# Performance work log

Measured on AMD Instinct MI355X. Metric: run time of the kernel, lower is better.

The kernel has to match this reference:

```python
import jax, jax.numpy as jnp
import numpy as np

T, B, D, H, F, E = 2048, 2, 1024, 16, 4096, 8
HD = D // H


def layer_norm(x, g, b, eps=1e-5):
    m = x.mean(-1, keepdims=True)
    v = ((x - m) ** 2).mean(-1, keepdims=True)
    return (x - m) * jax.lax.rsqrt(v + eps) * g + b


def setup_inputs() -> dict:
    key = jax.random.key(0)
    ks = jax.random.split(key, 24)
    s = 0.02
    inp = {
        "x": jax.random.normal(ks[0], (T, B, D), jnp.float32),
        # self-attention (fairseq MultiheadAttention)
        "Wq": jax.random.normal(ks[1], (D, D), jnp.float32) * s,
        "bq": jnp.zeros((D,), jnp.float32),
        "Wk": jax.random.normal(ks[2], (D, D), jnp.float32) * s,
        "bk": jnp.zeros((D,), jnp.float32),
        "Wv": jax.random.normal(ks[3], (D, D), jnp.float32) * s,
        "bv": jnp.zeros((D,), jnp.float32),
        "Wo": jax.random.normal(ks[4], (D, D), jnp.float32) * s,
        "bo": jnp.zeros((D,), jnp.float32),
        "ln1_g": jnp.ones((D,), jnp.float32),
        "ln1_b": jnp.zeros((D,), jnp.float32),
        "ln2_g": jnp.ones((D,), jnp.float32),
        "ln2_b": jnp.zeros((D,), jnp.float32),
        # MoE: expert_centroids Linear(D -> E, bias=False) => weight [E, D]
        "cent": jax.random.normal(ks[5], (E, D), jnp.float32) * s,
        # per-expert MoESublayer params (base_sublayers=1)
        "e_ln_g": jnp.ones((E, D), jnp.float32),
        "e_ln_b": jnp.zeros((E, D), jnp.float32),
        "e_W1": jax.random.normal(ks[6], (E, D, F), jnp.float32) * s,
        "e_b1": jnp.zeros((E, F), jnp.float32),
        "e_W2": jax.random.normal(ks[7], (E, F, D), jnp.float32) * s,
        "e_b2": jnp.zeros((E, D), jnp.float32),
    }
    return inp


def reference(x, Wq, bq, Wk, bk, Wv, bv, Wo, bo, ln1_g, ln1_b, ln2_g, ln2_b,
              cent, e_ln_g, e_ln_b, e_W1, e_b1, e_W2, e_b2):
    # ---- self-attention block (pre-norm, causal) ----
    res = x  # [T,B,D]
    h = layer_norm(x, ln1_g, ln1_b)
    q = ((h @ Wq) + bq) * (HD ** -0.5)
    k = h @ Wk + bk
    v = h @ Wv + bv
    q = q.reshape(T, B, H, HD)
    k = k.reshape(T, B, H, HD)
    v = v.reshape(T, B, H, HD)
    scores = jnp.einsum('tbhd,sbhd->bhts', q, k)
    causal = jnp.tril(jnp.ones((T, T), bool))
    scores = jnp.where(causal, scores, -1e9)
    p = jax.nn.softmax(scores, axis=-1)
    a = jnp.einsum('bhts,sbhd->tbhd', p, v).reshape(T, B, D)
    x = res + (a @ Wo + bo)

    # ---- MoE block (pre-norm) ----
    res = x
    h = layer_norm(x, ln2_g, ln2_b)
    # MoELayer: transpose(0,1) then flatten -> [B*T, D] token-major by batch
    xs = h.transpose(1, 0, 2).reshape(B * T, D)
    logits = xs.astype(jnp.float32) @ cent.T  # fp32 gating, [N,E]
    assign = jnp.argmax(logits, axis=-1)      # greedy top-1 routing

    # single-device semantics: All2All identity; sort + inverse-sort cancel,
    # so out[t] = expert_{assign[t]}(xs[t]). Compute each expert densely and select.
    def sublayer(g, b, W1, b1, W2, b2):
        hh = jax.nn.relu(layer_norm(xs, g, b) @ W1 + b1)  # [N,F]
        return xs + hh @ W2 + b2                          # internal residual

    ys = jax.vmap(sublayer)(e_ln_g, e_ln_b, e_W1, e_b1, e_W2, e_b2)  # [E,N,D]
    moe_out = jnp.take_along_axis(ys, assign[None, :, None], axis=0)[0]  # [N,D]
    moe_out = moe_out.reshape(B, T, D).transpose(1, 0, 2)  # back to [T,B,D]

    return res + moe_out
```

## Files before the change

kernel.cpp:

```cpp
#include <hip/hip_runtime.h>
#include <hip/hip_bf16.h>
#include <math.h>

#define T_ 2048
#define B_ 2
#define D_ 1024
#define H_ 16
#define F_ 4096
#define E_ 8
#define N_ 4096
#define HD_ 64
#define PADROWS 5120

typedef __attribute__((ext_vector_type(8))) short short8_t;
typedef __attribute__((ext_vector_type(4))) float f32x4_t;
typedef __attribute__((ext_vector_type(16))) float f32x16_t;
typedef __attribute__((ext_vector_type(4))) unsigned u32x4_t;

__device__ __forceinline__ unsigned short f2bf(float f) {
    union { float f; unsigned u; } a; a.f = f;
    unsigned r = a.u + 0x7FFFu + ((a.u >> 16) & 1u);
    return (unsigned short)(r >> 16);
}

__device__ __forceinline__ unsigned cvtpk(float lo, float hi) {
    unsigned r;
    asm("v_cvt_pk_bf16_f32 %0, %1, %2" : "=v"(r) : "v"(lo), "v"(hi));
    return r;
}

__device__ __forceinline__ void glds16(const unsigned short* g, unsigned short* l) {
    __builtin_amdgcn_global_load_lds(
        (const __attribute__((address_space(1))) void*)g,
        (__attribute__((address_space(3))) void*)l, 16, 0, 0);
}

__device__ __forceinline__ void blockReduce2(float& a, float& b, float* sm) {
    #pragma unroll
    for (int m = 32; m; m >>= 1) { a += __shfl_xor(a, m); b += __shfl_xor(b, m); }
    const int w = threadIdx.x >> 6, l = threadIdx.x & 63;
    __syncthreads();
    if (l == 0) { sm[w] = a; sm[8 + w] = b; }
    __syncthreads();
    a = sm[0] + sm[1] + sm[2] + sm[3];
    b = sm[8] + sm[9] + sm[10] + sm[11];
}

__global__ __launch_bounds__(256) void k_transpose(const float* __restrict__ in,
                                                   unsigned short* __restrict__ out,
                                                   int R, int C) {
    __shared__ float tile[32][33];
    const int c0 = blockIdx.x * 32, r0 = blockIdx.y * 32;
    const size_t base = (size_t)blockIdx.z * R * C;
    in += base; out += base;
    const int tx = threadIdx.x & 31, ty = threadIdx.x >> 5;
    #pragma unroll
    for (int i = 0; i < 32; i += 8)
        tile[ty + i][tx] = in[(size_t)(r0 + ty + i) * C + c0 + tx];
    __syncthreads();
    #pragma unroll
    for (int i = 0; i < 32; i += 8)
        out[(size_t)(c0 + ty + i) * R + r0 + tx] = f2bf(tile[tx][ty + i]);
}

__global__ __launch_bounds__(256) void k_transpose_v(const unsigned short* __restrict__ in,
                                                     unsigned short* __restrict__ out) {
    const int bh = blockIdx.x;
    const int t0 = blockIdx.y * 128;
    const int tid = threadIdx.x;
    const int hd = tid & 63;
    const size_t ib = (size_t)bh * T_ * HD_;
    const size_t ob = (size_t)bh * HD_ * T_;
    for (int tb = tid >> 6; tb < 16; tb += 4) {
        const int t = t0 + tb * 8;
        short8_t v;
        #pragma unroll
        for (int k = 0; k < 8; ++k)
            v[k] = (short)in[ib + (size_t)(t + k) * HD_ + hd];
        *(short8_t*)(out + ob + (size_t)hd * T_ + t) = v;
    }
}

__global__ __launch_bounds__(256) void k_ln(const float* __restrict__ x,
                                            const float* __restrict__ g,
                                            const float* __restrict__ b,
                                            unsigned short* __restrict__ out) {
    __shared__ float sm[16];
    const int row = blockIdx.x, tid = threadIdx.x;
    const float4 v = *(const float4*)(x + (size_t)row * D_ + tid * 4);
    float s1 = v.x + v.y + v.z + v.w;
    float s2 = v.x * v.x + v.y * v.y + v.z * v.z + v.w * v.w;
    blockReduce2(s1, s2, sm);
    const float mean = s1 * (1.f / D_);
    const float inv  = rsqrtf(s2 * (1.f / D_) - mean * mean + 1e-5f);
    const float4 gg = *(const float4*)(g + tid * 4);
    const float4 bb = *(const float4*)(b + tid * 4);
    unsigned long long pk =
          (unsigned long long)f2bf((v.x - mean) * inv * gg.x + bb.x)
        | ((unsigned long long)f2bf((v.y - mean) * inv * gg.y + bb.y) << 16)
        | ((unsigned long long)f2bf((v.z - mean) * inv * gg.z + bb.z) << 32)
        | ((unsigned long long)f2bf((v.w - mean) * inv * gg.w + bb.w) << 48);
    *(unsigned long long*)(out + (size_t)row * D_ + tid * 4) = pk;
}

__global__ __launch_bounds__(256) void k_init_x2(const float* __restrict__ x,
                                                 const float* __restrict__ bo,
                                                 float* __restrict__ x2) {
    const int row = blockIdx.x, tid = threadIdx.x;
    const size_t idx = (size_t)row * D_ + tid * 4;
    const float4 v = *(const float4*)(x + idx);
    const float4 b = *(const float4*)(bo + tid * 4);
    float4 o; o.x = v.x + b.x; o.y = v.y + b.y; o.z = v.z + b.z; o.w = v.w + b.w;
    *(float4*)(x2 + idx) = o;
}

__global__ __launch_bounds__(256) void k_init_out(const float* __restrict__ x2u,
                                                  const float* __restrict__ eb2,
                                                  const int* __restrict__ assign,
                                                  float* __restrict__ out) {
    const int row = blockIdx.x, tid = threadIdx.x;
    const int e = assign[row];
    const size_t idx = (size_t)row * D_ + tid * 4;
    const float4 v = *(const float4*)(x2u + idx);
    const float4 b = *(const float4*)(eb2 + (size_t)e * D_ + tid * 4);
    float4 o; o.x = v.x + b.x; o.y = v.y + b.y; o.z = v.z + b.z; o.w = v.w + b.w;
    *(float4*)(out + idx) = o;
}

__device__ __forceinline__ void gemm_core(const unsigned short* ap0, const unsigned short* ap1,
                                          const unsigned short* bp0, const unsigned short* bp1,
                                          int K, unsigned short* Als, unsigned short* Bls,
                                          f32x4_t (&acc)[4][4]) {
    const int tid = threadIdx.x, w = tid >> 6, l = tid & 63;
    const int wm = (w >> 1) * 64, wn = (w & 1) * 64;
    const int fr = l & 15, fg = (l >> 4) * 8;
    const int fgs = fg ^ (((fr >> 1) & 3) << 3);
    f32x4_t z4 = {0.f, 0.f, 0.f, 0.f};
    #pragma unroll
    for (int m = 0; m < 4; m++)
        #pragma unroll
        for (int n = 0; n < 4; n++) acc[m][n] = z4;
    glds16(ap0, Als + w * 512);
    glds16(ap1, Als + (w + 4) * 512);
    glds16(bp0, Bls + w * 512);
    glds16(bp1, Bls + (w + 4) * 512);
    ap0 += 32; ap1 += 32; bp0 += 32; bp1 += 32;
    glds16(ap0, Als + 4096 + w * 512);
    glds16(ap1, Als + 4096 + (w + 4) * 512);
    glds16(bp0, Bls + 4096 + w * 512);
    glds16(bp1, Bls + 4096 + (w + 4) * 512);
    ap0 += 32; ap1 += 32; bp0 += 32; bp1 += 32;
    unsigned c0 = 0, c1 = 4096, c2 = 8192;
    const int nk = K >> 5;
    for (int kt = 0; kt < nk; ++kt) {
        if (kt < nk - 1) asm volatile("s_waitcnt vmcnt(4)" ::: "memory");
        else             asm volatile("s_waitcnt vmcnt(0)" ::: "memory");
        __builtin_amdgcn_s_barrier();
        __builtin_amdgcn_sched_barrier(0);
        short8_t a[4], b[4];
        #pragma unroll
        for (int m = 0; m < 4; m++) a[m] = *(const short8_t*)(Als + c0 + (wm + m * 16 + fr) * 32 + fgs);
        #pragma unroll
        for (int n = 0; n < 4; n++) b[n] = *(const short8_t*)(Bls + c0 + (wn + n * 16 + fr) * 32 + fgs);
        #pragma unroll
        for (int m = 0; m < 4; m++)
            #pragma unroll
            for (int n = 0; n < 4; n++)
                acc[m][n] = __builtin_amdgcn_mfma_f32_16x16x32_bf16(a[m], b[n], acc[m][n], 0, 0, 0);
        if (kt + 2 < nk) {
            glds16(ap0, Als + c2 + w * 512);
            glds16(ap1, Als + c2 + (w + 4) * 512);
            glds16(bp0, Bls + c2 + w * 512);
            glds16(bp1, Bls + c2 + (w + 4) * 512);
            ap0 += 32; ap1 += 32; bp0 += 32; bp1 += 32;
        }
        const unsigned t = c0; c0 = c1; c1 = c2; c2 = t;
    }
}

__global__ __launch_bounds__(256) void k_gemm_qkv(
    const unsigned short* __restrict__ A, const unsigned short* __restrict__ BT,
    const float* __restrict__ bq, const float* __restrict__ bk, const float* __restrict__ bv,
    unsigned short* __restrict__ Qb, unsigned short* __restrict__ Kb, unsigned short* __restrict__ Vb) {
    __shared__ unsigned short Als[12288], Bls[12288];
    const int tid = threadIdx.x, w = tid >> 6, l = tid & 63;
    const int col0 = blockIdx.x * 128, row0 = blockIdx.y * 128;
    const int r0s = w * 16 + (l >> 2), r1s = 64 + w * 16 + (l >> 2);
    const int cs = ((l & 3) ^ ((l >> 3) & 3)) * 8;
    const unsigned short* ap0 = A + (size_t)(row0 + r0s) * D_ + cs;
    const unsigned short* ap1 = A + (size_t)(row0 + r1s) * D_ + cs;
    const unsigned short* bp0 = BT + (size_t)(col0 + r0s) * D_ + cs;
    const unsigned short* bp1 = BT + (size_t)(col0 + r1s) * D_ + cs;
    f32x4_t acc[4][4];
    gemm_core(ap0, ap1, bp0, bp1, D_, Als, Bls, acc);
    const int wm = (w >> 1) * 64, wn = (w & 1) * 64, fr = l & 15, fg4 = l >> 4;
    #pragma unroll
    for (int n = 0; n < 4; n++) {
        const int gcol = col0 + wn + n * 16 + fr;
        const int which = gcol >> 10, dc = gcol & 1023;
        const float bias = which == 0 ? bq[dc] : (which == 1 ? bk[dc] : bv[dc]);
        unsigned short* dst = which == 0 ? Qb : (which == 1 ? Kb : Vb);
        const int hh = dc >> 6, hd = dc & 63;
        #pragma unroll
        for (int m = 0; m < 4; m++)
            #pragma unroll
            for (int rr = 0; rr < 4; rr++) {
                const int grow = row0 + wm + m * 16 + fg4 * 4 + rr;
                float v = acc[m][n][rr] + bias;
                if (which == 0) v *= 0.1803368801111204f;
                const int t = grow >> 1, bb = grow & 1;
                dst[((size_t)(bb * H_ + hh) * T_ + t) * HD_ + hd] = f2bf(v);
            }
    }
}

__global__ __launch_bounds__(256) void k_attn(const unsigned short* __restrict__ Qb,
                                              const unsigned short* __restrict__ Kb,
                                              const unsigned short* __restrict__ Vt,
                                              unsigned short* __restrict__ aout) {
    __shared__ unsigned short Kl[2][4096];
    __shared__ unsigned short Vl[2][4096];
    const int id = blockIdx.x;
    const int qt = (id < 256) ? (15 - (id & 15)) : (id & 15);
    const int bh = (id >> 4) & 31;
    const int tid = threadIdx.x, w = tid >> 6, l = tid & 63;
    const int q5 = l & 31, hi = l >> 5, l7 = l & 7;
    const int row0 = w * 8 + (l >> 3);
    const int swz = ((l & 7) ^ (l >> 3)) * 8;
    const size_t base = (size_t)bh * T_ * HD_;
    const unsigned short* Qp = Qb + base;
    const unsigned short* kps = Kb + base + (size_t)row0 * HD_ + swz;
    const unsigned short* vps = Vt + base + (size_t)row0 * T_ + swz;
    const int qw0 = qt * 128 + w * 32;
    const int q = qw0 + q5;

    short8_t aq[4];
    #pragma unroll
    for (int khd = 0; khd < 4; ++khd)
        aq[khd] = *(const short8_t*)(Qp + (size_t)q * HD_ + khd * 16 + hi * 8);

    f32x16_t accO0, accO1;
    #pragma unroll
    for (int i = 0; i < 16; ++i) { accO0[i] = 0.f; accO1[i] = 0.f; }
    float mrun = -1e30f, lrun = 0.f;

    const int niter = (qt + 1) * 2;

    glds16(kps,            &Kl[0][w * 512]);
    glds16(kps + 32 * HD_, &Kl[0][2048 + w * 512]);
    glds16(vps,            &Vl[0][w * 512]);
    glds16(vps + 32 * T_,  &Vl[0][2048 + w * 512]);
    asm volatile("s_waitcnt vmcnt(0)" ::: "memory");
    __syncthreads();

    for (int it = 0; it < niter; ++it) {
        const int cur = it & 1;
        const int s0 = it * 64;
        if (it + 1 < niter) {
            const size_t ko = (size_t)(it + 1) * 64 * HD_;
            const int vo = (it + 1) * 64;
            glds16(kps + ko,            &Kl[cur ^ 1][w * 512]);
            glds16(kps + ko + 32 * HD_, &Kl[cur ^ 1][2048 + w * 512]);
            glds16(vps + vo,            &Vl[cur ^ 1][w * 512]);
            glds16(vps + vo + 32 * T_,  &Vl[cur ^ 1][2048 + w * 512]);
        }
        if (s0 <= qw0 + 31) {
            const unsigned short* KT = Kl[cur];
            const unsigned short* VT = Vl[cur];

            f32x16_t st0, st1;
            #pragma unroll
            for (int i = 0; i < 16; ++i) { st0[i] = 0.f; st1[i] = 0.f; }
            #pragma unroll
            for (int khd = 0; khd < 4; ++khd) {
                const int cb = (khd * 16 + hi * 8) ^ (l7 * 8);
                const short8_t k0 = *(const short8_t*)(KT + q5 * 64 + cb);
                const short8_t k1 = *(const short8_t*)(KT + (32 + q5) * 64 + cb);
                st0 = __builtin_amdgcn_mfma_f32_32x32x16_bf16(k0, aq[khd], st0, 0, 0, 0);
                st1 = __builtin_amdgcn_mfma_f32_32x32x16_bf16(k1, aq[khd], st1, 0, 0, 0);
            }

            const bool domask = (s0 + 63 > qw0);
            float pmax = -3e38f;
            #pragma unroll
            for (int r = 0; r < 16; ++r) {
                float v0 = st0[r], v1 = st1[r];
                if (domask) {
                    const int kv0 = s0 + (r & 3) + 8 * (r >> 2) + 4 * hi;
                    if (kv0 > q)      v0 = -1e30f;
                    if (kv0 + 32 > q) v1 = -1e30f;
                }
                st0[r] = v0; st1[r] = v1;
                pmax = fmaxf(pmax, fmaxf(v0, v1));
            }
            pmax = fmaxf(pmax, __shfl_xor(pmax, 32));
            const float mnew = fmaxf(mrun, pmax);
            const float scl = exp2f(mrun - mnew);
            float pt0[16], pt1[16];
            float rs = 0.f;
            #pragma unroll
            for (int r = 0; r < 16; ++r) {
                pt0[r] = exp2f(st0[r] - mnew);
                pt1[r] = exp2f(st1[r] - mnew);
                rs += pt0[r] + pt1[r];
            }
            rs += __shfl_xor(rs, 32);
            lrun = lrun * scl + rs;
            mrun = mnew;
            #pragma unroll
            for (int i = 0; i < 16; ++i) { accO0[i] *= scl; accO1[i] *= scl; }

            unsigned Wp[2][4][2];
            #pragma unroll
            for (int b = 0; b < 4; ++b) {
                Wp[0][b][0] = cvtpk(pt0[4 * b + 0], pt0[4 * b + 1]);
                Wp[0][b][1] = cvtpk(pt0[4 * b + 2], pt0[4 * b + 3]);
                Wp[1][b][0] = cvtpk(pt1[4 * b + 0], pt1[4 * b + 1]);
                Wp[1][b][1] = cvtpk(pt1[4 * b + 2], pt1[4 * b + 3]);
            }

            #pragma unroll
            for (int ks = 0; ks < 4; ++ks) {
                const int t = ks >> 1, b0 = (ks & 1) * 2;
                const unsigned ownA0 = Wp[t][b0][0],     ownA1 = Wp[t][b0][1];
                const unsigned ownB0 = Wp[t][b0 + 1][0], ownB1 = Wp[t][b0 + 1][1];
                const unsigned send0 = hi ? ownA0 : ownB0;
                const unsigned send1 = hi ? ownA1 : ownB1;
                const unsigned recv0 = __shfl_xor(send0, 32);
                const unsigned recv1 = __shfl_xor(send1, 32);
                u32x4_t wds;
                wds[0] = hi ? recv0 : ownA0;
                wds[1] = hi ? recv1 : ownA1;
                wds[2] = hi ? ownB0 : recv0;
                wds[3] = hi ? ownB1 : recv1;
                const short8_t pfrag = __builtin_bit_cast(short8_t, wds);
                const int cb = (ks * 16 + hi * 8) ^ (l7 * 8);
                const short8_t v0 = *(const short8_t*)(VT + q5 * 64 + cb);
                const short8_t v1 = *(const short8_t*)(VT + (32 + q5) * 64 + cb);
                accO0 = __builtin_amdgcn_mfma_f32_32x32x16_bf16(v0, pfrag, accO0, 0, 0, 0);
                accO1 = __builtin_amdgcn_mfma_f32_32x32x16_bf16(v1, pfrag, accO1, 0, 0, 0);
            }
        }
        asm volatile("s_waitcnt vmcnt(0)" ::: "memory");
        __syncthreads();
    }

    const float linv = 1.f / lrun;
    const int bidx = bh >> 4, hidx = bh & 15;
    unsigned short* orow = aout + (size_t)(q * B_ + bidx) * D_ + hidx * 64;
    #pragma unroll
    for (int g = 0; g < 4; ++g) {
        const int hd0 = 8 * g + 4 * hi;
        unsigned long long pk0 =
              (unsigned long long)f2bf(accO0[4 * g + 0] * linv)
            | ((unsigned long long)f2bf(accO0[4 * g + 1] * linv) << 16)
            | ((unsigned long long)f2bf(accO0[4 * g + 2] * linv) << 32)
            | ((unsigned long long)f2bf(accO0[4 * g + 3] * linv) << 48);
        *(unsigned long long*)(orow + hd0) = pk0;
        unsigned long long pk1 =
              (unsigned long long)f2bf(accO1[4 * g + 0] * linv)
            | ((unsigned long long)f2bf(accO1[4 * g + 1] * linv) << 16)
            | ((unsigned long long)f2bf(accO1[4 * g + 2] * linv) << 32)
            | ((unsigned long long)f2bf(accO1[4 * g + 3] * linv) << 48);
        *(unsigned long long*)(orow + 32 + hd0) = pk1;
    }
}

__global__ __launch_bounds__(256) void k_gemm_o(
    const unsigned short* __restrict__ A, const unsigned short* __restrict__ BT,
    float* __restrict__ x2) {
    __shared__ unsigned short Als[12288], Bls[12288];
    const int tid = threadIdx.x, w = tid >> 6, l = tid & 63;
    const int row0 = blockIdx.x * 128, col0 = blockIdx.y * 128;
    const int kc = blockIdx.z * 512;
    const int r0s = w * 16 + (l >> 2), r1s = 64 + w * 16 + (l >> 2);
    const int cs = ((l & 3) ^ ((l >> 3) & 3)) * 8;
    const unsigned short* ap0 = A + (size_t)(row0 + r0s) * D_ + kc + cs;
    const unsigned short* ap1 = A + (size_t)(row0 + r1s) * D_ + kc + cs;
    const unsigned short* bp0 = BT + (size_t)(col0 + r0s) * D_ + kc + cs;
    const unsigned short* bp1 = BT + (size_t)(col0 + r1s) * D_ + kc + cs;
    f32x4_t acc[4][4];
    gemm_core(ap0, ap1, bp0, bp1, 512, Als, Bls, acc);
    const int wm = (w >> 1) * 64, wn = (w & 1) * 64, fr = l & 15, fg4 = l >> 4;
    #pragma unroll
    for (int n = 0; n < 4; n++) {
        const int gcol = col0 + wn + n * 16 + fr;
        #pragma unroll
        for (int m = 0; m < 4; m++)
            #pragma unroll
            for (int rr = 0; rr < 4; rr++) {
                const int grow = row0 + wm + m * 16 + fg4 * 4 + rr;
                atomicAdd(&x2[(size_t)grow * D_ + gcol], acc[m][n][rr]);
            }
    }
}

__global__ __launch_bounds__(256) void k_ln2_gate(
    float* __restrict__ x2, const float* __restrict__ g2, const float* __restrict__ b2,
    const float* __restrict__ cent, const float* __restrict__ eg, const float* __restrict__ eb,
    unsigned short* __restrict__ z, int* __restrict__ assign, int* __restrict__ counts) {
    __shared__ float sm[48];
    const int row = blockIdx.x, tid = threadIdx.x;
    const int w = tid >> 6, l = tid & 63;
    float* xr = x2 + (size_t)row * D_;
    const float4 v = *(const float4*)(xr + tid * 4);
    float s1 = v.x + v.y + v.z + v.w;
    float s2 = v.x * v.x + v.y * v.y + v.z * v.z + v.w * v.w;
    blockReduce2(s1, s2, sm);
    const float mean = s1 * (1.f / D_);
    const float inv  = rsqrtf(s2 * (1.f / D_) - mean * mean + 1e-5f);
    const float4 gg = *(const float4*)(g2 + tid * 4), bb = *(const float4*)(b2 + tid * 4);
    float4 u;
    u.x = (v.x - mean) * inv * gg.x + bb.x;
    u.y = (v.y - mean) * inv * gg.y + bb.y;
    u.z = (v.z - mean) * inv * gg.z + bb.z;
    u.w = (v.w - mean) * inv * gg.w + bb.w;
    float p[E_];
    #pragma unroll
    for (int e = 0; e < E_; e++) {
        const float4 c = *(const float4*)(cent + (size_t)e * D_ + tid * 4);
        p[e] = u.x * c.x + u.y * c.y + u.z * c.z + u.w * c.w;
    }
    #pragma unroll
    for (int m = 32; m; m >>= 1)
        #pragma unroll
        for (int e = 0; e < E_; e++) p[e] += __shfl_xor(p[e], m);
    __syncthreads();
    if (l == 0) {
        #pragma unroll
        for (int e = 0; e < E_; e++) sm[16 + e * 4 + w] = p[e];
    }
    __syncthreads();
    int best = 0; float bl = -1e30f;
    #pragma unroll
    for (int e = 0; e < E_; e++) {
        const float le = sm[16 + e * 4] + sm[16 + e * 4 + 1] + sm[16 + e * 4 + 2] + sm[16 + e * 4 + 3];
        if (le > bl) { bl = le; best = e; }
    }
    float t1 = u.x + u.y + u.z + u.w;
    float t2 = u.x * u.x + u.y * u.y + u.z * u.z + u.w * u.w;
    blockReduce2(t1, t2, sm);
    const float m2   = t1 * (1.f / D_);
    const float inv2 = rsqrtf(t2 * (1.f / D_) - m2 * m2 + 1e-5f);
    const float4 egv = *(const float4*)(eg + (size_t)best * D_ + tid * 4);
    const float4 ebv = *(const float4*)(eb + (size_t)best * D_ + tid * 4);
    unsigned long long pk =
          (unsigned long long)f2bf((u.x - m2) * inv2 * egv.x + ebv.x)
        | ((unsigned long long)f2bf((u.y - m2) * inv2 * egv.y + ebv.y) << 16)
        | ((unsigned long long)f2bf((u.z - m2) * inv2 * egv.z + ebv.z) << 32)
        | ((unsigned long long)f2bf((u.w - m2) * inv2 * egv.w + ebv.w) << 48);
    *(unsigned long long*)(z + (size_t)row * D_ + tid * 4) = pk;
    float4 xu; xu.x = v.x + u.x; xu.y = v.y + u.y; xu.z = v.z + u.z; xu.w = v.w + u.w;
    *(float4*)(xr + tid * 4) = xu;
    if (tid == 0) { assign[row] = best; atomicAdd(&counts[best], 1); }
}

__global__ void k_init(int* counts, int* cursor, int* perm) {
    const int t = threadIdx.x;
    if (t < E_) { counts[t] = 0; cursor[t] = 0; }
    for (int i = t; i < PADROWS; i += 256) perm[i] = -1;
}

__global__ void k_offsets(const int* counts, int* pad_off) {
    if (threadIdx.x == 0) {
        int o = 0; pad_off[0] = 0;
        for (int e = 0; e < E_; e++) { o += ((counts[e] + 127) >> 7) << 7; pad_off[e + 1] = o; }
    }
}

__global__ void k_scatter(const int* assign, const int* pad_off, int* cursor, int* perm) {
    const int r = blockIdx.x * 256 + threadIdx.x;
    if (r >= N_) return;
    const int e = assign[r];
    const int pos = pad_off[e] + atomicAdd(&cursor[e], 1);
    perm[pos] = r;
}

__global__ __launch_bounds__(256) void k_gemm_e1(
    const unsigned short* __restrict__ z, const unsigned short* __restrict__ W1T,
    const float* __restrict__ eb1, const int* __restrict__ pad_off,
    const int* __restrict__ perm, unsigned short* __restrict__ Y1) {
    __shared__ unsigned short Als[12288], Bls[12288];
    const int tid = threadIdx.x, w = tid >> 6, l = tid & 63;
    const int col0 = blockIdx.x * 128, row0 = blockIdx.y * 128;
    if (row0 >= pad_off[E_]) return;
    int e = 0;
    while (row0 >= pad_off[e + 1]) e++;
    const int r0s = w * 16 + (l >> 2), r1s = 64 + w * 16 + (l >> 2);
    const int cs = ((l & 3) ^ ((l >> 3) & 3)) * 8;
    int pr0 = perm[row0 + r0s]; if (pr0 < 0) pr0 = 0;
    int pr1 = perm[row0 + r1s]; if (pr1 < 0) pr1 = 0;
    const unsigned short* ap0 = z + (size_t)pr0 * D_ + cs;
    const unsigned short* ap1 = z + (size_t)pr1 * D_ + cs;
    const unsigned short* BTe = W1T + (size_t)e * F_ * D_;
    const unsigned short* bp0 = BTe + (size_t)(col0 + r0s) * D_ + cs;
    const unsigned short* bp1 = BTe + (size_t)(col0 + r1s) * D_ + cs;
    f32x4_t acc[4][4];
    gemm_core(ap0, ap1, bp0, bp1, D_, Als, Bls, acc);
    const float* b1e = eb1 + (size_t)e * F_;
    const int wm = (w >> 1) * 64, wn = (w & 1) * 64, fr = l & 15, fg4 = l >> 4;
    #pragma unroll
    for (int n = 0; n < 4; n++) {
        const int gcol = col0 + wn + n * 16 + fr;
        const float bias = b1e[gcol];
        #pragma unroll
        for (int m = 0; m < 4; m++)
            #pragma unroll
            for (int rr = 0; rr < 4; rr++) {
                const int grow = row0 + wm + m * 16 + fg4 * 4 + rr;
                Y1[(size_t)grow * F_ + gcol] = f2bf(fmaxf(acc[m][n][rr] + bias, 0.f));
            }
    }
}

__global__ __launch_bounds__(256) void k_gemm_e2(
    const unsigned short* __restrict__ Y1, const unsigned short* __restrict__ W2T,
    const int* __restrict__ pad_off, const int* __restrict__ perm,
    float* __restrict__ out) {
    __shared__ unsigned short Als[12288], Bls[12288];
    const int tid = threadIdx.x, w = tid >> 6, l = tid & 63;
    const int row0 = blockIdx.x * 128, col0 = blockIdx.y * 128;
    const int kc = blockIdx.z * 2048;
    if (row0 >= pad_off[E_]) return;
    int e = 0;
    while (row0 >= pad_off[e + 1]) e++;
    const int r0s = w * 16 + (l >> 2), r1s = 64 + w * 16 + (l >> 2);
    const int cs = ((l & 3) ^ ((l >> 3) & 3)) * 8;
    const unsigned short* ap0 = Y1 + (size_t)(row0 + r0s) * F_ + kc + cs;
    const unsigned short* ap1 = Y1 + (size_t)(row0 + r1s) * F_ + kc + cs;
    const unsigned short* BTe = W2T + (size_t)e * D_ * F_;
    const unsigned short* bp0 = BTe + (size_t)(col0 + r0s) * F_ + kc + cs;
    const unsigned short* bp1 = BTe + (size_t)(col0 + r1s) * F_ + kc + cs;
    f32x4_t acc[4][4];
    gemm_core(ap0, ap1, bp0, bp1, 2048, Als, Bls, acc);
    const int wm = (w >> 1) * 64, wn = (w & 1) * 64, fr = l & 15, fg4 = l >> 4;
    #pragma unroll
    for (int n = 0; n < 4; n++) {
        const int gcol = col0 + wn + n * 16 + fr;
        #pragma unroll
        for (int m = 0; m < 4; m++)
            #pragma unroll
            for (int rr = 0; rr < 4; rr++) {
                const int grow = row0 + wm + m * 16 + fg4 * 4 + rr;
                const int rdst = perm[grow];
                if (rdst >= 0)
                    atomicAdd(&out[(size_t)rdst * D_ + gcol], acc[m][n][rr]);
            }
    }
}

extern "C" void kernel_launch(void* const* d_in, const int* in_sizes, int n_in,
                              void* d_out, int out_size, void* d_ws, size_t ws_size,
                              hipStream_t stream) {
    const float* x    = (const float*)d_in[0];
    const float* Wq   = (const float*)d_in[1];
    const float* bq   = (const float*)d_in[2];
    const float* Wk   = (const float*)d_in[3];
    const float* bk   = (const float*)d_in[4];
    const float* Wv   = (const float*)d_in[5];
    const float* bv   = (const float*)d_in[6];
    const float* Wo   = (const float*)d_in[7];
    const float* bo   = (const float*)d_in[8];
    const float* ln1g = (const float*)d_in[9];
    const float* ln1b = (const float*)d_in[10];
    const float* ln2g = (const float*)d_in[11];
    const float* ln2b = (const float*)d_in[12];
    const float* cent = (const float*)d_in[13];
    const float* egw  = (const float*)d_in[14];
    const float* ebw  = (const float*)d_in[15];
    const float* eW1  = (const float*)d_in[16];
    const float* eb1  = (const float*)d_in[17];
    const float* eW2  = (const float*)d_in[18];
    const float* eb2  = (const float*)d_in[19];
    float* out = (float*)d_out;

    char* W = (char*)d_ws;
    unsigned short* WqkvT = (unsigned short*)(W);
    unsigned short* WoT   = (unsigned short*)(W + 6291456);
    unsigned short* Qb    = (unsigned short*)(W + 8388608);
    unsigned short* Kb    = (unsigned short*)(W + 16777216);
    unsigned short* Vb    = (unsigned short*)(W + 25165824);
    unsigned short* aout  = (unsigned short*)(W + 33554432);
    unsigned short* Y1    = (unsigned short*)(W);
    unsigned short* W1T   = (unsigned short*)(W + 41943040);
    unsigned short* W2T   = (unsigned short*)(W + 109051904);
    unsigned short* h1z   = (unsigned short*)(W + 176160768);
    float*          x2    = (float*)(W + 184549376);
    unsigned short* Vt    = (unsigned short*)(W + 201326592);
    int*            assign= (int*)(W + 209715200);
    int*            perm  = (int*)(W + 209731584);
    int*            counts= (int*)(W + 209752064);
    int*            cursor= (int*)(W + 209752192);
    int*            pad_off=(int*)(W + 209752320);

    k_transpose<<<dim3(32, 32, 1), 256, 0, stream>>>(Wq, WqkvT,               1024, 1024);
    k_transpose<<<dim3(32, 32, 1), 256, 0, stream>>>(Wk, WqkvT + 1024 * 1024, 1024, 1024);
    k_transpose<<<dim3(32, 32, 1), 256, 0, stream>>>(Wv, WqkvT + 2048 * 1024, 1024, 1024);
    k_transpose<<<dim3(32, 32, 1), 256, 0, stream>>>(Wo, WoT,                 1024, 1024);
    k_transpose<<<dim3(128, 32, 8), 256, 0, stream>>>(eW1, W1T, 1024, 4096);
    k_transpose<<<dim3(32, 128, 8), 256, 0, stream>>>(eW2, W2T, 4096, 1024);

    k_init<<<1, 256, 0, stream>>>(counts, cursor, perm);
    k_ln<<<N_, 256, 0, stream>>>(x, ln1g, ln1b, h1z);
    k_init_x2<<<N_, 256, 0, stream>>>(x, bo, x2);
    k_gemm_qkv<<<dim3(24, 32), 256, 0, stream>>>(h1z, WqkvT, bq, bk, bv, Qb, Kb, Vb);
    k_transpose_v<<<dim3(32, 16), 256, 0, stream>>>(Vb, Vt);
    k_attn<<<dim3(512), 256, 0, stream>>>(Qb, Kb, Vt, aout);
    k_gemm_o<<<dim3(32, 8, 2), 256, 0, stream>>>(aout, WoT, x2);
    k_ln2_gate<<<N_, 256, 0, stream>>>(x2, ln2g, ln2b, cent, egw, ebw, h1z, assign, counts);
    k_offsets<<<1, 64, 0, stream>>>(counts, pad_off);
    k_scatter<<<16, 256, 0, stream>>>(assign, pad_off, cursor, perm);
    k_init_out<<<N_, 256, 0, stream>>>(x2, eb2, assign, out);
    k_gemm_e1<<<dim3(32, 40), 256, 0, stream>>>(h1z, W1T, eb1, pad_off, perm, Y1);
    k_gemm_e2<<<dim3(40, 8, 2), 256, 0, stream>>>(Y1, W2T, pad_off, perm, out);
}
```

Before: 490.7 us.

## Triple-buffer K/V tiles in attention and vectorize transpose stores

The attention kernel moves from double to triple buffering of K/V tiles in shared memory. Loads are issued two iterations ahead, and it waits with a partial vmcnt and a single barrier per iteration instead of a full drain plus barrier. The aim is to hide global-to-LDS latency behind the MFMA work. Separately, the weight transpose kernel now writes 4 bf16 values per thread as one ushort4 store instead of scalar stores. The extra shared memory (48KB per block) may reduce how many attention blocks fit on each CU.

```diff
diff --git a/kernel.cpp b/kernel.cpp
--- a/kernel.cpp
+++ b/kernel.cpp
@@ -58,9 +58,13 @@
     for (int i = 0; i < 32; i += 8)
         tile[ty + i][tx] = in[(size_t)(r0 + ty + i) * C + c0 + tx];
     __syncthreads();
-    #pragma unroll
-    for (int i = 0; i < 32; i += 8)
-        out[(size_t)(c0 + ty + i) * R + r0 + tx] = f2bf(tile[tx][ty + i]);
+    const int c = threadIdx.x >> 3, rq = (threadIdx.x & 7) * 4;
+    ushort4 v;
+    v.x = f2bf(tile[rq + 0][c]);
+    v.y = f2bf(tile[rq + 1][c]);
+    v.z = f2bf(tile[rq + 2][c]);
+    v.w = f2bf(tile[rq + 3][c]);
+    *(ushort4*)(out + (size_t)(c0 + c) * R + r0 + rq) = v;
 }
 
 __global__ __launch_bounds__(256) void k_transpose_v(const unsigned short* __restrict__ in,
@@ -218,8 +222,8 @@
                                               const unsigned short* __restrict__ Kb,
                                               const unsigned short* __restrict__ Vt,
                                               unsigned short* __restrict__ aout) {
-    __shared__ unsigned short Kl[2][4096];
-    __shared__ unsigned short Vl[2][4096];
+    __shared__ unsigned short Kl[3 * 4096];
+    __shared__ unsigned short Vl[3 * 4096];
     const int id = blockIdx.x;
     const int qt = (id < 256) ? (15 - (id & 15)) : (id & 15);
     const int bh = (id >> 4) & 31;
@@ -246,27 +250,26 @@
 
     const int niter = (qt + 1) * 2;
 
-    glds16(kps,            &Kl[0][w * 512]);
-    glds16(kps + 32 * HD_, &Kl[0][2048 + w * 512]);
-    glds16(vps,            &Vl[0][w * 512]);
-    glds16(vps + 32 * T_,  &Vl[0][2048 + w * 512]);
-    asm volatile("s_waitcnt vmcnt(0)" ::: "memory");
-    __syncthreads();
+#define STAGE_KV(t, b) { \
+    const size_t ko = (size_t)(t) * 64 * HD_; const int vo = (t) * 64; \
+    glds16(kps + ko,            Kl + (b) + w * 512); \
+    glds16(kps + ko + 32 * HD_, Kl + (b) + 2048 + w * 512); \
+    glds16(vps + vo,            Vl + (b) + w * 512); \
+    glds16(vps + vo + 32 * T_,  Vl + (b) + 2048 + w * 512); }
+
+    STAGE_KV(0, 0);
+    STAGE_KV(1, 4096);
+    unsigned c0 = 0, c1 = 4096, c2 = 8192;
 
     for (int it = 0; it < niter; ++it) {
-        const int cur = it & 1;
+        if (it < niter - 1) asm volatile("s_waitcnt vmcnt(4)" ::: "memory");
+        else                asm volatile("s_waitcnt vmcnt(0)" ::: "memory");
+        __builtin_amdgcn_s_barrier();
+        __builtin_amdgcn_sched_barrier(0);
         const int s0 = it * 64;
-        if (it + 1 < niter) {
-            const size_t ko = (size_t)(it + 1) * 64 * HD_;
-            const int vo = (it + 1) * 64;
-            glds16(kps + ko,            &Kl[cur ^ 1][w * 512]);
-            glds16(kps + ko + 32 * HD_, &Kl[cur ^ 1][2048 + w * 512]);
-            glds16(vps + vo,            &Vl[cur ^ 1][w * 512]);
-            glds16(vps + vo + 32 * T_,  &Vl[cur ^ 1][2048 + w * 512]);
-        }
         if (s0 <= qw0 + 31) {
-            const unsigned short* KT = Kl[cur];
-            const unsigned short* VT = Vl[cur];
+            const unsigned short* KT = Kl + c0;
+            const unsigned short* VT = Vl + c0;
 
             f32x16_t st0, st1;
             #pragma unroll
@@ -341,9 +344,10 @@
                 accO1 = __builtin_amdgcn_mfma_f32_32x32x16_bf16(v1, pfrag, accO1, 0, 0, 0);
             }
         }
-        asm volatile("s_waitcnt vmcnt(0)" ::: "memory");
-        __syncthreads();
-    }
+        if (it + 2 < niter) STAGE_KV(it + 2, c2);
+        const unsigned tb = c0; c0 = c1; c1 = c2; c2 = tb;
+    }
+#undef STAGE_KV
 
     const float linv = 1.f / lrun;
     const int bidx = bh >> 4, hidx = bh & 15;
```

New measurement: 486.8 us. Within noise of the previous version (-0.8%).
